# Performance work log

Hardware: AMD Instinct MI355X
Metric: run time of the kernel (lower is better)

Reference implementation:

```python
import jax, jax.numpy as jnp
import numpy as np

B, S, D = 2, 2048, 1024
H, HD = 16, 64          # num_heads, head_dim
K = 32                  # JL n_components


def setup_inputs() -> dict:
    key = jax.random.key(0)
    k1, k2, k3, k4 = jax.random.split(key, 4)
    return {
        "hidden_states": jax.random.normal(k1, (B, S, D), dtype=jnp.float32),
        "W_attn": jax.random.normal(k2, (D, 3 * D), dtype=jnp.float32) * 0.02,
        "b_attn": jnp.zeros((3 * D,), dtype=jnp.float32),
        "S_proj": jax.random.normal(k3, (K, HD), dtype=jnp.float32) / np.sqrt(K),
        "W_proj": jax.random.normal(k4, (D, D), dtype=jnp.float32) * 0.02,
        "b_proj": jnp.zeros((D,), dtype=jnp.float32),
    }


def reference(hidden_states, W_attn, b_attn, S_proj, W_proj, b_proj):
    b, s, d = hidden_states.shape
    # GPT2 Conv1D: x @ W + b, then split into q,k,v
    qkv = hidden_states @ W_attn + b_attn            # [B,S,3D]
    q, k, v = jnp.split(qkv, 3, axis=-1)
    # split heads -> [B,H,S,HD]
    def split_heads(x):
        return x.reshape(b, s, H, HD).transpose(0, 2, 1, 3)
    q = split_heads(q) @ S_proj.T                    # [B,H,S,K] JL-reduced
    k = split_heads(k) @ S_proj.T                    # [B,H,S,K]
    v = split_heads(v)                               # [B,H,S,HD]
    # naive attention: scale by sqrt(value head_dim) per GPT2 _attn
    scores = jnp.einsum("bhqk,bhsk->bhqs", q, k) / jnp.sqrt(
        jnp.asarray(HD, dtype=v.dtype))              # [B,H,S,S]
    causal = jnp.tril(jnp.ones((s, s), dtype=bool))
    mask_value = jnp.finfo(scores.dtype).min
    scores = jnp.where(causal, scores, mask_value)
    attn = jax.nn.softmax(scores, axis=-1)
    out = jnp.einsum("bhqs,bhsd->bhqd", attn, v)     # [B,H,S,HD]
    out = out.transpose(0, 2, 1, 3).reshape(b, s, d)  # merge heads
    return out @ W_proj + b_proj
```

## Files before the change

kernel.cpp:

```cpp
#include <hip/hip_runtime.h>
#include <hip/hip_bf16.h>
#include <stdint.h>

#define B_ 2
#define S_ 2048
#define D_ 1024
#define H_ 16
#define HD_ 64
#define KJL 32
#define N3 3072
#define N2 2048

typedef __attribute__((ext_vector_type(8))) __bf16 bf16x8;
typedef __attribute__((ext_vector_type(4))) float floatx4;
typedef __attribute__((ext_vector_type(4))) short short4v;
typedef __attribute__((ext_vector_type(2))) unsigned int uint2v;

__device__ __forceinline__ unsigned short f2b(float x) {
  union { float f; unsigned u; } v; v.f = x;
  unsigned r = v.u + 0x7fffu + ((v.u >> 16) & 1u);
  return (unsigned short)(r >> 16);
}

__device__ __forceinline__ unsigned int pkbf(float lo, float hi) {
  union { float f; unsigned u; } a, b;
  a.f = lo; b.f = hi;
  return __builtin_amdgcn_perm(b.u + 0x8000u, a.u + 0x8000u, 0x07060302u);
}

__device__ __forceinline__ void async16(const void* g, void* l) {
  __builtin_amdgcn_global_load_lds((__attribute__((address_space(1))) void*)(g),
                                   (__attribute__((address_space(3))) void*)(l),
                                   16, 0, 0);
}

__global__ __launch_bounds__(256)
void prep_kernel(const float* __restrict__ hidden, unsigned short* __restrict__ hB,
                 const float* __restrict__ W_attn, const float* __restrict__ b_attn,
                 const float* __restrict__ Sp, const float* __restrict__ W_proj,
                 unsigned short* __restrict__ Bt2, unsigned short* __restrict__ WpT,
                 float* __restrict__ bias2) {
  __shared__ float shmem[2048];
  const int bid = blockIdx.x;
  const int tid = threadIdx.x;

  if (bid < 512) {
    const int n4 = (B_ * S_ * D_) / 4;
    int i = bid * 256 + tid;
    for (; i < n4; i += 512 * 256) {
      float4 v = *(const float4*)(hidden + 4 * (size_t)i);
      short4v o = {(short)f2b(v.x), (short)f2b(v.y), (short)f2b(v.z), (short)f2b(v.w)};
      *(short4v*)(hB + 4 * (size_t)i) = o;
    }
  } else if (bid < 2560) {
    const float* in;
    unsigned short* out;
    int Cs, local;
    if (bid < 1536) { local = bid - 512;  in = W_attn + 2048; out = Bt2 + 1024 * 1024; Cs = N3; }
    else            { local = bid - 1536; in = W_proj;        out = WpT;               Cs = D_; }
    float (*t)[33] = (float(*)[33])shmem;
    int c0 = (local & 31) * 32, r0 = (local >> 5) * 32;
    int tx = tid & 31, ty = tid >> 5;
    for (int j = 0; j < 32; j += 8)
      t[ty + j][tx] = in[(size_t)(r0 + ty + j) * Cs + c0 + tx];
    __syncthreads();
    for (int j = 0; j < 32; j += 8)
      out[(size_t)(c0 + ty + j) * D_ + r0 + tx] = f2b(t[tx][ty + j]);
  } else {
    const int lb = bid - 2560;
    const int part = lb >> 6;
    const int h = (lb >> 2) & 15;
    const int dc = lb & 3;
    for (int i = tid; i < 32 * 64; i += 256) shmem[i] = Sp[i];
    __syncthreads();
    const float scale = part ? 1.0f : 0.125f * 1.44269504f;
    const int d = dc * 256 + tid;
    float w[64];
    const float* src = W_attn + (size_t)d * N3 + part * D_ + h * 64;
    for (int j = 0; j < 16; ++j) {
      float4 v = *(const float4*)&src[j * 4];
      w[j * 4 + 0] = v.x; w[j * 4 + 1] = v.y; w[j * 4 + 2] = v.z; w[j * 4 + 3] = v.w;
    }
    const int nbase = part * 512 + h * 32;
    for (int kjl = 0; kjl < 32; ++kjl) {
      float acc = 0.f;
      for (int hd = 0; hd < 64; ++hd) acc += w[hd] * shmem[kjl * 64 + hd];
      Bt2[(size_t)(nbase + kjl) * D_ + d] = f2b(acc * scale);
    }
    if (dc == 0 && tid < 32) {
      float acc = 0.f;
      for (int hd = 0; hd < 64; ++hd) acc += b_attn[part * D_ + h * 64 + hd] * shmem[tid * 64 + hd];
      bias2[nbase + tid] = acc * scale;
    }
  }
}

__global__ __launch_bounds__(256, 2)
void qkv2_gemm_kernel(const unsigned short* __restrict__ A,
                      const unsigned short* __restrict__ Bt,
                      const float* __restrict__ b_attn,
                      const float* __restrict__ bias2,
                      unsigned short* __restrict__ Qjl,
                      unsigned short* __restrict__ Kjl,
                      unsigned short* __restrict__ Vc) {
  __shared__ __align__(16) unsigned short As[2][128 * 32];
  __shared__ __align__(16) unsigned short Bs[2][128 * 32];
  const int tid = threadIdx.x;
  const int lane = tid & 63, wv = tid >> 6;
  const int quad = lane >> 4, col = lane & 15;
  const int wm = wv >> 1, wn = wv & 1;
  const int m0 = blockIdx.y * 128, n0 = blockIdx.x * 128;

  floatx4 acc[4][4] = {};

  for (int kk = 0; kk < D_; kk += 64) {
    for (int it = 0; it < 4; ++it) {
      int c = it * 256 + tid;
      int ks = c >> 9, row = (c >> 2) & 127, kc = c & 3;
      async16(A + (size_t)(m0 + row) * D_ + kk + ks * 32 + kc * 8,
              (unsigned short*)As + c * 8);
    }
    for (int it = 0; it < 4; ++it) {
      int c = it * 256 + tid;
      int ks = c >> 9, row = (c >> 2) & 127, kc = c & 3;
      async16(Bt + (size_t)(n0 + row) * D_ + kk + ks * 32 + kc * 8,
              (unsigned short*)Bs + c * 8);
    }
    asm volatile("s_waitcnt vmcnt(0)" ::: "memory");
    __syncthreads();
    for (int ks = 0; ks < 2; ++ks) {
      bf16x8 af[4], bfr[4];
      for (int mt = 0; mt < 4; ++mt)
        af[mt] = *(const bf16x8*)&As[ks][(wm * 64 + mt * 16 + col) * 32 + quad * 8];
      for (int nt = 0; nt < 4; ++nt)
        bfr[nt] = *(const bf16x8*)&Bs[ks][(wn * 64 + nt * 16 + col) * 32 + quad * 8];
      for (int mt = 0; mt < 4; ++mt)
        for (int nt = 0; nt < 4; ++nt)
          acc[mt][nt] = __builtin_amdgcn_mfma_f32_16x16x32_bf16(
              af[mt], bfr[nt], acc[mt][nt], 0, 0, 0);
    }
    __syncthreads();
  }

  const int pq = n0 >> 9;
  for (int mt = 0; mt < 4; ++mt) {
    int gm0 = m0 + wm * 64 + mt * 16 + quad * 4;
    int b = gm0 >> 11, s = gm0 & (S_ - 1);
    for (int nt = 0; nt < 4; ++nt) {
      int gn = n0 + wn * 64 + nt * 16 + col;
      if (pq >= 2) {
        int vcol = gn - 1024;
        float bs = b_attn[2048 + vcol];
        int h = vcol >> 6, hd = vcol & 63;
        short4v vv;
        for (int i = 0; i < 4; ++i)
          vv[i] = (short)f2b(acc[mt][nt][i] + bs);
        size_t idx = ((((size_t)(b * H_ + h) * 64 + (s >> 5)) * 64 + hd) * 32 + (s & 31));
        *(short4v*)&Vc[idx] = vv;
      } else {
        float bs = bias2[gn];
        int gl = gn & 511;
        int h = gl >> 5, kjl = gl & 31;
        unsigned short* dst = pq ? Kjl : Qjl;
        size_t base = ((size_t)(b * H_ + h) * S_ + s) * KJL + kjl;
        for (int i = 0; i < 4; ++i)
          dst[base + (size_t)i * KJL] = f2b(acc[mt][nt][i] + bs);
      }
    }
  }
}

__global__ __launch_bounds__(256, 2)
void attn_kernel(const unsigned short* __restrict__ Qjl,
                 const unsigned short* __restrict__ Kjl,
                 const unsigned short* __restrict__ Vc,
                 unsigned short* __restrict__ AO) {
  __shared__ __align__(16) unsigned short Ps[4][32 * 136];
  const int tid = threadIdx.x;
  const int lane = tid & 63, wv = tid >> 6;
  const int quad = lane >> 4, l15 = lane & 15;

  const int blk = blockIdx.x;
  const int bh = blk & 31;
  const int t = blk >> 5;
  const int b = bh >> 4, h = bh & 15;

  unsigned short* Pw = &Ps[wv][0];
  const int nch = (t >> 2) + 1;
  const int kb = (wv * nch) >> 2;
  const int ke = ((wv + 1) * nch) >> 2;
  const int lastc = nch - 1;
  const int r = t & 3;

  const int laneK = l15 * KJL + quad * 8;
  const int laneV = l15 * 32 + quad * 8;
  const unsigned short* Kp = Kjl + (size_t)bh * S_ * KJL + laneK + (size_t)kb * 128 * KJL;
  const unsigned short* Vp = Vc + (size_t)bh * (64 * 64 * 32) + laneV + (size_t)kb * 8192;

  bf16x8 aq[2];
  for (int qn = 0; qn < 2; ++qn)
    aq[qn] = *(const bf16x8*)&Qjl[(size_t)(bh * S_ + t * 32 + qn * 16 + l15) * KJL + quad * 8];

  floatx4 o[4][2] = {};
  floatx4 psum[2] = {};
  const floatx4 zz = {0.f, 0.f, 0.f, 0.f};

  for (int kt = kb; kt < ke; ++kt) {
    bf16x8 ak[8];
    for (int sm = 0; sm < 8; ++sm)
      ak[sm] = *(const bf16x8*)&Kp[sm * (16 * KJL)];
    bf16x8 bv[4][4];
    for (int ks = 0; ks < 4; ++ks)
      for (int md = 0; md < 4; ++md)
        bv[ks][md] = *(const bf16x8*)&Vp[ks * 2048 + md * 512];
    Kp += 128 * KJL;
    Vp += 8192;

    floatx4 sc[8][2];
    __builtin_amdgcn_s_setprio(1);
    for (int sm = 0; sm < 8; ++sm)
      for (int qn = 0; qn < 2; ++qn)
        sc[sm][qn] = __builtin_amdgcn_mfma_f32_16x16x32_bf16(ak[sm], aq[qn], zz, 0, 0, 0);
    __builtin_amdgcn_s_setprio(0);

    if (kt == lastc) {
      for (int qn = 0; qn < 2; ++qn) {
        int qloc = r * 32 + qn * 16 + l15;
        for (int sm = 0; sm < 8; ++sm)
          for (int i = 0; i < 4; ++i)
            if (sm * 16 + quad * 4 + i > qloc) sc[sm][qn][i] = -1e30f;
      }
    }

    for (int qn = 0; qn < 2; ++qn) {
      for (int sm = 0; sm < 8; ++sm) {
        float p0 = __builtin_amdgcn_exp2f(sc[sm][qn][0]);
        float p1 = __builtin_amdgcn_exp2f(sc[sm][qn][1]);
        float p2 = __builtin_amdgcn_exp2f(sc[sm][qn][2]);
        float p3 = __builtin_amdgcn_exp2f(sc[sm][qn][3]);
        psum[qn][0] += p0; psum[qn][1] += p1;
        psum[qn][2] += p2; psum[qn][3] += p3;
        uint2v pk2 = {pkbf(p0, p1), pkbf(p2, p3)};
        *(uint2v*)&Pw[(qn * 16 + l15) * 136 + sm * 16 + quad * 4] = pk2;
      }
    }

    for (int ks = 0; ks < 4; ++ks) {
      bf16x8 bp[2];
      for (int qn = 0; qn < 2; ++qn)
        bp[qn] = *(const bf16x8*)&Pw[(qn * 16 + l15) * 136 + ks * 32 + quad * 8];
      __builtin_amdgcn_s_setprio(1);
      for (int qn = 0; qn < 2; ++qn)
        for (int md = 0; md < 4; ++md)
          o[md][qn] = __builtin_amdgcn_mfma_f32_16x16x32_bf16(bv[ks][md], bp[qn], o[md][qn], 0, 0, 0);
      __builtin_amdgcn_s_setprio(0);
    }
  }

  float l0 = psum[0][0] + psum[0][1] + psum[0][2] + psum[0][3];
  float l1 = psum[1][0] + psum[1][1] + psum[1][2] + psum[1][3];
  l0 += __shfl_xor(l0, 16, 64); l0 += __shfl_xor(l0, 32, 64);
  l1 += __shfl_xor(l1, 16, 64); l1 += __shfl_xor(l1, 32, 64);

  if (wv) {
    float* fp = (float*)Pw;
    for (int qn = 0; qn < 2; ++qn)
      for (int md = 0; md < 4; ++md)
        *(floatx4*)(fp + (qn * 4 + md) * 256 + lane * 4) = o[md][qn];
    fp[2048 + lane] = l0;
    fp[2112 + lane] = l1;
  }
  __syncthreads();

  if (!wv) {
    for (int p = 1; p < 4; ++p) {
      const float* fq = (const float*)(&Ps[p][0]);
      l0 += fq[2048 + lane];
      l1 += fq[2112 + lane];
      for (int qn = 0; qn < 2; ++qn)
        for (int md = 0; md < 4; ++md)
          o[md][qn] += *(const floatx4*)(fq + (qn * 4 + md) * 256 + lane * 4);
    }
    float inv0 = 1.f / l0;
    float inv1 = 1.f / l1;
    for (int qn = 0; qn < 2; ++qn) {
      float inv = qn ? inv1 : inv0;
      for (int md = 0; md < 4; ++md) {
        floatx4 s = o[md][qn];
        uint2v t4 = {pkbf(s[0] * inv, s[1] * inv),
                     pkbf(s[2] * inv, s[3] * inv)};
        *(uint2v*)&Pw[(qn * 16 + l15) * 72 + md * 16 + quad * 4] = t4;
      }
    }
    asm volatile("s_waitcnt lgkmcnt(0)" ::: "memory");
    int q = lane >> 1, hf = lane & 1;
    size_t gbase = ((size_t)(b * S_ + t * 32 + q)) * D_ + h * HD_ + hf * 32;
    for (int jj = 0; jj < 4; ++jj) {
      bf16x8 v = *(const bf16x8*)&Pw[q * 72 + hf * 32 + jj * 8];
      *(bf16x8*)&AO[gbase + jj * 8] = v;
    }
  }
}

__global__ __launch_bounds__(256, 2)
void proj_gemm_kernel(const unsigned short* __restrict__ A,
                      const unsigned short* __restrict__ Bt,
                      const float* __restrict__ bias,
                      float* __restrict__ out) {
  __shared__ __align__(16) unsigned short As[2][64 * 32];
  __shared__ __align__(16) unsigned short Bs[2][128 * 32];
  const int tid = threadIdx.x;
  const int lane = tid & 63, wv = tid >> 6;
  const int quad = lane >> 4, col = lane & 15;
  const int wm = wv >> 1, wn = wv & 1;
  const int m0 = blockIdx.y * 64, n0 = blockIdx.x * 128;

  floatx4 acc[2][4] = {};

  for (int kk = 0; kk < D_; kk += 64) {
    for (int it = 0; it < 2; ++it) {
      int c = it * 256 + tid;
      int ks = c >> 8, row = (c >> 2) & 63, kc = c & 3;
      async16(A + (size_t)(m0 + row) * D_ + kk + ks * 32 + kc * 8,
              (unsigned short*)As + c * 8);
    }
    for (int it = 0; it < 4; ++it) {
      int c = it * 256 + tid;
      int ks = c >> 9, row = (c >> 2) & 127, kc = c & 3;
      async16(Bt + (size_t)(n0 + row) * D_ + kk + ks * 32 + kc * 8,
              (unsigned short*)Bs + c * 8);
    }
    asm volatile("s_waitcnt vmcnt(0)" ::: "memory");
    __syncthreads();
    for (int ks = 0; ks < 2; ++ks) {
      bf16x8 af[2], bfr[4];
      for (int mt = 0; mt < 2; ++mt)
        af[mt] = *(const bf16x8*)&As[ks][(wm * 32 + mt * 16 + col) * 32 + quad * 8];
      for (int nt = 0; nt < 4; ++nt)
        bfr[nt] = *(const bf16x8*)&Bs[ks][(wn * 64 + nt * 16 + col) * 32 + quad * 8];
      for (int mt = 0; mt < 2; ++mt)
        for (int nt = 0; nt < 4; ++nt)
          acc[mt][nt] = __builtin_amdgcn_mfma_f32_16x16x32_bf16(
              af[mt], bfr[nt], acc[mt][nt], 0, 0, 0);
    }
    __syncthreads();
  }

  for (int mt = 0; mt < 2; ++mt) {
    int gm0 = m0 + wm * 32 + mt * 16 + quad * 4;
    for (int nt = 0; nt < 4; ++nt) {
      int gn = n0 + wn * 64 + nt * 16 + col;
      float bs = bias[gn];
      for (int i = 0; i < 4; ++i)
        out[(size_t)(gm0 + i) * D_ + gn] = acc[mt][nt][i] + bs;
    }
  }
}

extern "C" void kernel_launch(void* const* d_in, const int* in_sizes, int n_in,
                              void* d_out, int out_size, void* d_ws, size_t ws_size,
                              hipStream_t stream) {
  (void)in_sizes; (void)n_in; (void)out_size; (void)ws_size;
  const float* hidden = (const float*)d_in[0];
  const float* W_attn = (const float*)d_in[1];
  const float* b_attn = (const float*)d_in[2];
  const float* S_proj = (const float*)d_in[3];
  const float* W_proj = (const float*)d_in[4];
  const float* b_proj = (const float*)d_in[5];
  float* out = (float*)d_out;

  char* ws = (char*)d_ws;
  unsigned short* hB    = (unsigned short*)(ws);
  unsigned short* Bt2   = (unsigned short*)(ws + (8u << 20));
  unsigned short* WpT   = (unsigned short*)(ws + (12u << 20));
  float*          bias2 = (float*)         (ws + (14u << 20));
  unsigned short* Qjl   = (unsigned short*)(ws + (15u << 20));
  unsigned short* Kjl   = (unsigned short*)(ws + (19u << 20));
  unsigned short* Vc    = (unsigned short*)(ws + (23u << 20));
  unsigned short* AO    = (unsigned short*)(ws + (31u << 20));

  prep_kernel<<<2688, 256, 0, stream>>>(hidden, hB, W_attn, b_attn, S_proj,
                                        W_proj, Bt2, WpT, bias2);
  qkv2_gemm_kernel<<<dim3(N2 / 128, (B_ * S_) / 128), 256, 0, stream>>>(
      hB, Bt2, b_attn, bias2, Qjl, Kjl, Vc);
  attn_kernel<<<2048, 256, 0, stream>>>(Qjl, Kjl, Vc, AO);
  proj_gemm_kernel<<<dim3(D_ / 128, (B_ * S_) / 64), 256, 0, stream>>>(
      AO, WpT, b_proj, out);
}
```

Before: 181.5 us.

## Share double-buffered K/V chunks across waves in attention, one query tile per wave

The attention kernel now gives each workgroup four consecutive 32-query tiles, one per wave, instead of splitting one tile's KV range across four waves. K/V chunks are staged into LDS with async copies and double buffering, so all four waves reuse the same data. This removes the cross-wave partial-sum reduction at the end of the kernel. It also adds an XOR swizzle on the P scratch to reduce LDS bank conflicts, and pairs causal tile groups to balance work. The trade-offs are a 4x smaller grid, more LDS per block, and a barrier on every chunk iteration.

```diff
diff --git a/kernel.cpp b/kernel.cpp
--- a/kernel.cpp
+++ b/kernel.cpp
@@ -175,27 +175,27 @@
                  const unsigned short* __restrict__ Kjl,
                  const unsigned short* __restrict__ Vc,
                  unsigned short* __restrict__ AO) {
-  __shared__ __align__(16) unsigned short Ps[4][32 * 136];
+  __shared__ __align__(16) unsigned short Kb[2][4096];
+  __shared__ __align__(16) unsigned short Vb[2][8192];
+  __shared__ __align__(16) unsigned short Ps[4][4096];
   const int tid = threadIdx.x;
   const int lane = tid & 63, wv = tid >> 6;
   const int quad = lane >> 4, l15 = lane & 15;
 
   const int blk = blockIdx.x;
   const int bh = blk & 31;
-  const int t = blk >> 5;
+  const int gg = (blk >> 5) & 7;
+  const int g = (blk >> 8) ? (15 - gg) : gg;
+  const int t = g * 4 + wv;
   const int b = bh >> 4, h = bh & 15;
-
-  unsigned short* Pw = &Ps[wv][0];
-  const int nch = (t >> 2) + 1;
-  const int kb = (wv * nch) >> 2;
-  const int ke = ((wv + 1) * nch) >> 2;
+  const int nch = g + 1;
   const int lastc = nch - 1;
-  const int r = t & 3;
-
-  const int laneK = l15 * KJL + quad * 8;
-  const int laneV = l15 * 32 + quad * 8;
-  const unsigned short* Kp = Kjl + (size_t)bh * S_ * KJL + laneK + (size_t)kb * 128 * KJL;
-  const unsigned short* Vp = Vc + (size_t)bh * (64 * 64 * 32) + laneV + (size_t)kb * 8192;
+
+  const unsigned short* Kg = Kjl + (size_t)bh * S_ * KJL;
+  const unsigned short* Vg = Vc + (size_t)bh * (64 * 64 * 32);
+
+  char* Pw = (char*)&Ps[wv][0];
+  const int pswz = l15 << 4;
 
   bf16x8 aq[2];
   for (int qn = 0; qn < 2; ++qn)
@@ -205,16 +205,33 @@
   floatx4 psum[2] = {};
   const floatx4 zz = {0.f, 0.f, 0.f, 0.f};
 
-  for (int kt = kb; kt < ke; ++kt) {
+#define STAGE(bu, c) do {                                                   \
+    const char* ks_ = (const char*)(Kg + (size_t)(c) * 4096);               \
+    const char* vs_ = (const char*)(Vg + (size_t)(c) * 8192);               \
+    char* kd_ = (char*)&Kb[bu][0];                                          \
+    char* vd_ = (char*)&Vb[bu][0];                                          \
+    async16(ks_ + tid * 16,         kd_ + tid * 16);                        \
+    async16(ks_ + tid * 16 + 4096,  kd_ + tid * 16 + 4096);                 \
+    async16(vs_ + tid * 16,         vd_ + tid * 16);                        \
+    async16(vs_ + tid * 16 + 4096,  vd_ + tid * 16 + 4096);                 \
+    async16(vs_ + tid * 16 + 8192,  vd_ + tid * 16 + 8192);                 \
+    async16(vs_ + tid * 16 + 12288, vd_ + tid * 16 + 12288);                \
+  } while (0)
+
+  STAGE(0, 0);
+  asm volatile("s_waitcnt vmcnt(0)" ::: "memory");
+  __syncthreads();
+
+  int cur = 0;
+  for (int kt = 0; kt < nch; ++kt) {
+    if (kt + 1 < nch) STAGE(cur ^ 1, kt + 1);
+
+    const char* Kc = (const char*)&Kb[cur][0];
+    const char* Vl = (const char*)&Vb[cur][0];
+
     bf16x8 ak[8];
     for (int sm = 0; sm < 8; ++sm)
-      ak[sm] = *(const bf16x8*)&Kp[sm * (16 * KJL)];
-    bf16x8 bv[4][4];
-    for (int ks = 0; ks < 4; ++ks)
-      for (int md = 0; md < 4; ++md)
-        bv[ks][md] = *(const bf16x8*)&Vp[ks * 2048 + md * 512];
-    Kp += 128 * KJL;
-    Vp += 8192;
+      ak[sm] = *(const bf16x8*)(Kc + (sm * 16 + l15) * 64 + quad * 16);
 
     floatx4 sc[8][2];
     __builtin_amdgcn_s_setprio(1);
@@ -225,7 +242,7 @@
 
     if (kt == lastc) {
       for (int qn = 0; qn < 2; ++qn) {
-        int qloc = r * 32 + qn * 16 + l15;
+        int qloc = wv * 32 + qn * 16 + l15;
         for (int sm = 0; sm < 8; ++sm)
           for (int i = 0; i < 4; ++i)
             if (sm * 16 + quad * 4 + i > qloc) sc[sm][qn][i] = -1e30f;
@@ -241,46 +258,37 @@
         psum[qn][0] += p0; psum[qn][1] += p1;
         psum[qn][2] += p2; psum[qn][3] += p3;
         uint2v pk2 = {pkbf(p0, p1), pkbf(p2, p3)};
-        *(uint2v*)&Pw[(qn * 16 + l15) * 136 + sm * 16 + quad * 4] = pk2;
+        *(uint2v*)(Pw + (qn * 16 + l15) * 256 + ((sm * 32 + quad * 8) ^ pswz)) = pk2;
       }
     }
 
     for (int ks = 0; ks < 4; ++ks) {
+      bf16x8 bv[4];
+      for (int md = 0; md < 4; ++md)
+        bv[md] = *(const bf16x8*)(Vl + ks * 4096 + md * 1024 + l15 * 64 + quad * 16);
       bf16x8 bp[2];
       for (int qn = 0; qn < 2; ++qn)
-        bp[qn] = *(const bf16x8*)&Pw[(qn * 16 + l15) * 136 + ks * 32 + quad * 8];
+        bp[qn] = *(const bf16x8*)(Pw + (qn * 16 + l15) * 256 + ((ks * 64 + quad * 16) ^ pswz));
       __builtin_amdgcn_s_setprio(1);
       for (int qn = 0; qn < 2; ++qn)
         for (int md = 0; md < 4; ++md)
-          o[md][qn] = __builtin_amdgcn_mfma_f32_16x16x32_bf16(bv[ks][md], bp[qn], o[md][qn], 0, 0, 0);
+          o[md][qn] = __builtin_amdgcn_mfma_f32_16x16x32_bf16(bv[md], bp[qn], o[md][qn], 0, 0, 0);
       __builtin_amdgcn_s_setprio(0);
     }
-  }
+
+    asm volatile("s_waitcnt vmcnt(0)" ::: "memory");
+    __syncthreads();
+    cur ^= 1;
+  }
+#undef STAGE
 
   float l0 = psum[0][0] + psum[0][1] + psum[0][2] + psum[0][3];
   float l1 = psum[1][0] + psum[1][1] + psum[1][2] + psum[1][3];
   l0 += __shfl_xor(l0, 16, 64); l0 += __shfl_xor(l0, 32, 64);
   l1 += __shfl_xor(l1, 16, 64); l1 += __shfl_xor(l1, 32, 64);
 
-  if (wv) {
-    float* fp = (float*)Pw;
-    for (int qn = 0; qn < 2; ++qn)
-      for (int md = 0; md < 4; ++md)
-        *(floatx4*)(fp + (qn * 4 + md) * 256 + lane * 4) = o[md][qn];
-    fp[2048 + lane] = l0;
-    fp[2112 + lane] = l1;
-  }
-  __syncthreads();
-
-  if (!wv) {
-    for (int p = 1; p < 4; ++p) {
-      const float* fq = (const float*)(&Ps[p][0]);
-      l0 += fq[2048 + lane];
-      l1 += fq[2112 + lane];
-      for (int qn = 0; qn < 2; ++qn)
-        for (int md = 0; md < 4; ++md)
-          o[md][qn] += *(const floatx4*)(fq + (qn * 4 + md) * 256 + lane * 4);
-    }
+  {
+    unsigned short* Pu = (unsigned short*)Pw;
     float inv0 = 1.f / l0;
     float inv1 = 1.f / l1;
     for (int qn = 0; qn < 2; ++qn) {
@@ -289,14 +297,14 @@
         floatx4 s = o[md][qn];
         uint2v t4 = {pkbf(s[0] * inv, s[1] * inv),
                      pkbf(s[2] * inv, s[3] * inv)};
-        *(uint2v*)&Pw[(qn * 16 + l15) * 72 + md * 16 + quad * 4] = t4;
+        *(uint2v*)&Pu[(qn * 16 + l15) * 72 + md * 16 + quad * 4] = t4;
       }
     }
     asm volatile("s_waitcnt lgkmcnt(0)" ::: "memory");
     int q = lane >> 1, hf = lane & 1;
     size_t gbase = ((size_t)(b * S_ + t * 32 + q)) * D_ + h * HD_ + hf * 32;
     for (int jj = 0; jj < 4; ++jj) {
-      bf16x8 v = *(const bf16x8*)&Pw[q * 72 + hf * 32 + jj * 8];
+      bf16x8 v = *(const bf16x8*)&Pu[q * 72 + hf * 32 + jj * 8];
       *(bf16x8*)&AO[gbase + jj * 8] = v;
     }
   }
@@ -383,7 +391,7 @@
                                         W_proj, Bt2, WpT, bias2);
   qkv2_gemm_kernel<<<dim3(N2 / 128, (B_ * S_) / 128), 256, 0, stream>>>(
       hB, Bt2, b_attn, bias2, Qjl, Kjl, Vc);
-  attn_kernel<<<2048, 256, 0, stream>>>(Qjl, Kjl, Vc, AO);
+  attn_kernel<<<512, 256, 0, stream>>>(Qjl, Kjl, Vc, AO);
   proj_gemm_kernel<<<dim3(D_ / 128, (B_ * S_) / 64), 256, 0, stream>>>(
       AO, WpT, b_proj, out);
 }
```

After: 179.1 us. About the same (-1.3%).
